# Optimization experiments

Hardware: AMD Instinct MI355X
Metric: run time of the kernel (lower is better)

The kernel has to match this reference:

```python
import jax, jax.numpy as jnp
import numpy as np

B, L, D, H, F, NL, K, G = 2, 2048, 768, 12, 3072, 12, 128, 16
HD = D // H
SCALE = HD ** -0.5


def setup_inputs() -> dict:
    key = jax.random.key(0)
    ks = jax.random.split(key, 8)
    n = lambda k, s, std=0.02: jax.random.normal(k, s, dtype=jnp.float32) * std
    return {
        "x": jax.random.normal(ks[0], (B, L, D), dtype=jnp.float32),
        "pos_conv_w": n(ks[1], (D, D // G, K)),
        "pos_conv_b": jnp.zeros((D,), jnp.float32),
        "ln0_g": jnp.ones((D,), jnp.float32), "ln0_b": jnp.zeros((D,), jnp.float32),
        "Wq": n(ks[2], (NL, D, D)), "bq": jnp.zeros((NL, D), jnp.float32),
        "Wk": n(ks[3], (NL, D, D)), "bk": jnp.zeros((NL, D), jnp.float32),
        "Wv": n(ks[4], (NL, D, D)), "bv": jnp.zeros((NL, D), jnp.float32),
        "Wo": n(ks[5], (NL, D, D)), "bo": jnp.zeros((NL, D), jnp.float32),
        "ln1_g": jnp.ones((NL, D), jnp.float32), "ln1_b": jnp.zeros((NL, D), jnp.float32),
        "W1": n(ks[6], (NL, D, F)), "b1": jnp.zeros((NL, F), jnp.float32),
        "W2": n(ks[7], (NL, F, D)), "b2": jnp.zeros((NL, D), jnp.float32),
        "ln2_g": jnp.ones((NL, D), jnp.float32), "ln2_b": jnp.zeros((NL, D), jnp.float32),
    }


def _ln(x, g, b, eps=1e-5):
    m = jnp.mean(x, axis=-1, keepdims=True)
    v = jnp.mean(jnp.square(x - m), axis=-1, keepdims=True)
    return (x - m) * jax.lax.rsqrt(v + eps) * g + b


def reference(x, pos_conv_w, pos_conv_b, ln0_g, ln0_b, Wq, bq, Wk, bk, Wv, bv, Wo, bo,
              ln1_g, ln1_b, W1, b1, W2, b2, ln2_g, ln2_b):
    b_, l_, d_ = x.shape
    # positional grouped conv embedding (kernel even -> drop last frame), GELU, residual add
    pos = jax.lax.conv_general_dilated(x.transpose(0, 2, 1), pos_conv_w, (1,), [(K // 2, K // 2)],
                                       feature_group_count=G)  # (B, D, L+1)
    pos = pos[:, :, :l_] + pos_conv_b[None, :, None]
    h = x + jax.nn.gelu(pos, approximate=False).transpose(0, 2, 1)
    # post-norm encoder (layer_norm_first=False): LN applied before the layer stack
    h = _ln(h, ln0_g, ln0_b)

    def layer(h, p):
        wq, bq_, wk, bk_, wv, bv_, wo, bo_, g1, be1, w1, bf1, w2, bf2, g2, be2 = p
        r = h
        q = (h @ wq + bq_).reshape(b_, l_, H, HD)
        k = (h @ wk + bk_).reshape(b_, l_, H, HD)
        v = (h @ wv + bv_).reshape(b_, l_, H, HD)
        w = jax.nn.softmax(SCALE * jnp.einsum('blhd,bmhd->bhlm', q, k), axis=-1)
        o = jnp.einsum('bhlm,bmhd->blhd', w, v).reshape(b_, l_, d_)
        h = r + (o @ wo + bo_)
        h = _ln(h, g1, be1)
        ff = jax.nn.gelu(h @ w1 + bf1, approximate=False) @ w2 + bf2
        h = _ln(h + ff, g2, be2)
        return h, None

    h, _ = jax.lax.scan(layer, h, (Wq, bq, Wk, bk, Wv, bv, Wo, bo,
                                   ln1_g, ln1_b, W1, b1, W2, b2, ln2_g, ln2_b))
    return h
```

## Files before the change

### kernel.cpp

```cpp
#include <hip/hip_runtime.h>
#include <hip/hip_bf16.h>
#include <stdint.h>

#define B_ 2
#define L_ 2048
#define D_ 768
#define H_ 12
#define F_ 3072
#define NL_ 12
#define K_ 128
#define G_ 16
#define HD_ 64
#define CPG_ 48
#define M_TOK (B_*L_)
#define SCALE_ 0.125f

typedef __hip_bfloat16 bf16;
typedef __bf16 bf16x8 __attribute__((ext_vector_type(8)));
typedef float f32x4 __attribute__((ext_vector_type(4)));

__device__ __forceinline__ void gload16(const void* g, void* l) {
  __builtin_amdgcn_global_load_lds((const __attribute__((address_space(1))) void*)g,
                                   (__attribute__((address_space(3))) void*)l, 16, 0, 0);
}

__global__ __launch_bounds__(256) void convw_kernel(const float* __restrict__ w,
                                                    bf16* __restrict__ wT2) {
  int idx = blockIdx.x * 256 + threadIdx.x;
  int ci = idx & 63;
  int row = idx >> 6;
  int d = row % 48;
  int t2 = row / 48;
  int kk = t2 & 127;
  int g = t2 >> 7;
  float v = (ci < 48) ? w[(((size_t)(g * 48 + d) * 48) + ci) * 128 + kk] : 0.f;
  wT2[idx] = __float2bfloat16(v);
}

__global__ __launch_bounds__(256) void conv_mfma(const float* __restrict__ x,
                                                 const bf16* __restrict__ wT2,
                                                 const float* __restrict__ bias,
                                                 float* __restrict__ out) {
  int flat = blockIdx.x;
  int wgid = (flat & 7) * 64 + (flat >> 3);
  const int g = wgid >> 5;
  int rem = wgid & 31;
  const int l0 = (rem & 15) * 128;
  const int b = rem >> 4;

  const int tid = threadIdx.x, w = tid >> 6, lane = tid & 63;
  const int c15 = lane & 15, g4 = lane >> 4;
  __shared__ __align__(16) bf16 win[256 * 64];
  __shared__ __align__(16) bf16 Wl[2 * 48 * 64];

  {
    int lg = l0 - 64 + tid;
    char* dst = (char*)win + tid * 128;
    int swr = (tid & 7) << 4;
    uint4 z4 = {0u, 0u, 0u, 0u};
    if ((unsigned)lg < 2048u) {
      const float* srow = x + ((size_t)(b * 2048 + lg) * 768 + g * 48);
#pragma unroll
      for (int c = 0; c < 6; ++c) {
        float4 v0 = *(const float4*)(srow + c * 8);
        float4 v1 = *(const float4*)(srow + c * 8 + 4);
        union { bf16 h[8]; uint4 u; } uu;
        uu.h[0] = __float2bfloat16(v0.x); uu.h[1] = __float2bfloat16(v0.y);
        uu.h[2] = __float2bfloat16(v0.z); uu.h[3] = __float2bfloat16(v0.w);
        uu.h[4] = __float2bfloat16(v1.x); uu.h[5] = __float2bfloat16(v1.y);
        uu.h[6] = __float2bfloat16(v1.z); uu.h[7] = __float2bfloat16(v1.w);
        *(uint4*)(dst + ((c * 16) ^ swr)) = uu.u;
      }
    } else {
#pragma unroll
      for (int c = 0; c < 6; ++c) *(uint4*)(dst + ((c * 16) ^ swr)) = z4;
    }
    *(uint4*)(dst + (96 ^ swr)) = z4;
    *(uint4*)(dst + (112 ^ swr)) = z4;
  }
  __syncthreads();

  f32x4 acc[2][3];
  const f32x4 vzero = {0.f, 0.f, 0.f, 0.f};
#pragma unroll
  for (int i = 0; i < 2; ++i)
#pragma unroll
    for (int j = 0; j < 3; ++j) acc[i][j] = vzero;

  const char* wbase = (const char*)wT2 + (size_t)g * 128 * 48 * 128;

  for (int kp = 0; kp < 64; ++kp) {
#pragma unroll
    for (int i = 0; i < 3; ++i) {
      int coff = w * 3072 + i * 1024;
      int c = coff + (lane << 4);
      int row96 = c >> 7;
      int s = row96 / 48;
      int d = row96 - s * 48;
      int cb2 = c & 127;
      gload16(wbase + ((size_t)((2 * kp + s) * 48 + d)) * 128 + (cb2 ^ ((d & 7) << 4)),
              (char*)Wl + coff);
    }
    __syncthreads();
#pragma unroll
    for (int s = 0; s < 2; ++s) {
      int kk = 2 * kp + s;
#pragma unroll
      for (int cb = 0; cb < 2; ++cb) {
        int a0r = w * 16 + c15 + kk;
        int a1r = 64 + a0r;
        bf16x8 a0 = *(const bf16x8*)((const char*)win + a0r * 128 + ((cb * 64 + g4 * 16) ^ ((a0r & 7) << 4)));
        bf16x8 a1 = *(const bf16x8*)((const char*)win + a1r * 128 + ((cb * 64 + g4 * 16) ^ ((a1r & 7) << 4)));
#pragma unroll
        for (int ct = 0; ct < 3; ++ct) {
          int d = ct * 16 + c15;
          bf16x8 bfrag = *(const bf16x8*)((const char*)Wl + s * 6144 + d * 128 +
                                          ((cb * 64 + g4 * 16) ^ ((d & 7) << 4)));
          acc[0][ct] = __builtin_amdgcn_mfma_f32_16x16x32_bf16(a0, bfrag, acc[0][ct], 0, 0, 0);
          acc[1][ct] = __builtin_amdgcn_mfma_f32_16x16x32_bf16(a1, bfrag, acc[1][ct], 0, 0, 0);
        }
      }
    }
    __syncthreads();
  }

#pragma unroll
  for (int ls = 0; ls < 2; ++ls)
#pragma unroll
    for (int ct = 0; ct < 3; ++ct) {
      int dg = g * 48 + ct * 16 + c15;
      float bv = bias[dg];
#pragma unroll
      for (int r = 0; r < 4; ++r) {
        int l = l0 + ls * 64 + w * 16 + g4 * 4 + r;
        size_t idx = (size_t)(b * 2048 + l) * 768 + dg;
        float vv = acc[ls][ct][r] + bv;
        vv = 0.5f * vv * (1.0f + erff(vv * 0.70710678f));
        out[idx] = x[idx] + vv;
      }
    }
}

__global__ __launch_bounds__(256) void ln_kernel(const float* __restrict__ a,
                                                 const float* __restrict__ r,
                                                 const float* __restrict__ g,
                                                 const float* __restrict__ be,
                                                 float* __restrict__ out,
                                                 bf16* __restrict__ outb) {
  int w = threadIdx.x >> 6, lane = threadIdx.x & 63;
  size_t row = (size_t)blockIdx.x * 4 + w;
  const float* ar = a + row * 768;
  const float* rr = r ? r + row * 768 : nullptr;
  float4 v[3];
  float s = 0.f;
#pragma unroll
  for (int i = 0; i < 3; ++i) {
    int c = lane * 4 + i * 256;
    float4 vv = *(const float4*)(ar + c);
    if (rr) {
      float4 rv = *(const float4*)(rr + c);
      vv.x += rv.x; vv.y += rv.y; vv.z += rv.z; vv.w += rv.w;
    }
    v[i] = vv;
    s += vv.x + vv.y + vv.z + vv.w;
  }
#pragma unroll
  for (int st = 1; st < 64; st <<= 1) s += __shfl_xor(s, st);
  float mean = s * (1.0f / 768.0f);
  float s2 = 0.f;
#pragma unroll
  for (int i = 0; i < 3; ++i) {
    float dx = v[i].x - mean, dy = v[i].y - mean, dz = v[i].z - mean, dw = v[i].w - mean;
    s2 += dx * dx + dy * dy + dz * dz + dw * dw;
  }
#pragma unroll
  for (int st = 1; st < 64; st <<= 1) s2 += __shfl_xor(s2, st);
  float rstd = rsqrtf(s2 * (1.0f / 768.0f) + 1e-5f);
#pragma unroll
  for (int i = 0; i < 3; ++i) {
    int c = lane * 4 + i * 256;
    float4 gv = *(const float4*)(g + c);
    float4 bv = *(const float4*)(be + c);
    float4 ov;
    ov.x = (v[i].x - mean) * rstd * gv.x + bv.x;
    ov.y = (v[i].y - mean) * rstd * gv.y + bv.y;
    ov.z = (v[i].z - mean) * rstd * gv.z + bv.z;
    ov.w = (v[i].w - mean) * rstd * gv.w + bv.w;
    *(float4*)(out + row * 768 + c) = ov;
    if (outb) {
      union { bf16 h[4]; uint2 u; } pk;
      pk.h[0] = __float2bfloat16(ov.x); pk.h[1] = __float2bfloat16(ov.y);
      pk.h[2] = __float2bfloat16(ov.z); pk.h[3] = __float2bfloat16(ov.w);
      *(uint2*)(outb + row * 768 + c) = pk.u;
    }
  }
}

__global__ __launch_bounds__(256) void prep_weights(const float* __restrict__ wq,
                                                    const float* __restrict__ wk,
                                                    const float* __restrict__ wv,
                                                    const float* __restrict__ wo,
                                                    const float* __restrict__ w1,
                                                    const float* __restrict__ w2,
                                                    const float* __restrict__ bq_,
                                                    const float* __restrict__ bk_,
                                                    const float* __restrict__ bv_,
                                                    bf16* __restrict__ wqkvb,
                                                    bf16* __restrict__ wob,
                                                    bf16* __restrict__ w1b,
                                                    bf16* __restrict__ w2b,
                                                    float* __restrict__ bqkv) {
  __shared__ float t[32][33];
  int tid = threadIdx.x;
  int tx = tid & 31, ty = tid >> 5;
  int blk = blockIdx.x;
  if (blk >= 6912) {
    int i = (blk - 6912) * 256 + tid;
    if (i < 2304) bqkv[i] = (i < 768) ? bq_[i] : (i < 1536) ? bk_[i - 768] : bv_[i - 1536];
    return;
  }
  if (blk < 1728) {
    int n0 = (blk % 72) * 32, k0 = (blk / 72) * 32;
    const float* src = (n0 < 768) ? wq : (n0 < 1536) ? wk : wv;
    int nn = (n0 >= 1536) ? (n0 - 1536) : (n0 >= 768 ? n0 - 768 : n0);
#pragma unroll
    for (int i = 0; i < 32; i += 8) t[ty + i][tx] = src[(size_t)(k0 + ty + i) * 768 + nn + tx];
    __syncthreads();
#pragma unroll
    for (int i = 0; i < 32; i += 8)
      wqkvb[(size_t)(n0 + ty + i) * 768 + k0 + tx] = __float2bfloat16(t[tx][ty + i]);
    return;
  }
  blk -= 1728;
  if (blk < 576) {
    int c0 = (blk % 24) * 32, r0 = (blk / 24) * 32;
#pragma unroll
    for (int i = 0; i < 32; i += 8) t[ty + i][tx] = wo[(size_t)(r0 + ty + i) * 768 + c0 + tx];
    __syncthreads();
#pragma unroll
    for (int i = 0; i < 32; i += 8)
      wob[(size_t)(c0 + ty + i) * 768 + r0 + tx] = __float2bfloat16(t[tx][ty + i]);
    return;
  }
  blk -= 576;
  if (blk < 2304) {
    int c0 = (blk % 96) * 32, r0 = (blk / 96) * 32;
#pragma unroll
    for (int i = 0; i < 32; i += 8) t[ty + i][tx] = w1[(size_t)(r0 + ty + i) * 3072 + c0 + tx];
    __syncthreads();
#pragma unroll
    for (int i = 0; i < 32; i += 8)
      w1b[(size_t)(c0 + ty + i) * 768 + r0 + tx] = __float2bfloat16(t[tx][ty + i]);
    return;
  }
  blk -= 2304;
  {
    int c0 = (blk % 24) * 32, r0 = (blk / 24) * 32;
#pragma unroll
    for (int i = 0; i < 32; i += 8) t[ty + i][tx] = w2[(size_t)(r0 + ty + i) * 768 + c0 + tx];
    __syncthreads();
#pragma unroll
    for (int i = 0; i < 32; i += 8)
      w2b[(size_t)(c0 + ty + i) * 3072 + r0 + tx] = __float2bfloat16(t[tx][ty + i]);
  }
}

template <int BM, int BN, int GELU, int BF16OUT, int VOUT = 0>
__global__ __launch_bounds__(256) void gemm_bf16(const bf16* __restrict__ A,
                                                 const bf16* __restrict__ BT,
                                                 const float* __restrict__ bias,
                                                 void* __restrict__ Cout,
                                                 int N, int Kd,
                                                 bf16* __restrict__ vTout = nullptr) {
  constexpr int WM = BM / 2, MF = WM / 16;
  constexpr int WN = BN / 2, FN = WN / 16;
  __shared__ bf16 As[BM * 64];
  __shared__ bf16 Bs[BN * 64];
  const int tid = threadIdx.x, w = tid >> 6, lane = tid & 63;
  int gx = gridDim.x;
  int flat = blockIdx.x + gx * blockIdx.y;
  int cpx = (gx * gridDim.y) >> 3;
  int sw = (flat & 7) * cpx + (flat >> 3);
  const int bn = sw % gx, bm = sw / gx;
  const int wr = w >> 1, wc = w & 1;
  const int c15 = lane & 15, g4 = lane >> 4;
  const int lrow8 = lane >> 3;
  const int cb = (lane & 7) * 16;

  f32x4 acc[MF][FN];
  const f32x4 vzero = {0.f, 0.f, 0.f, 0.f};
#pragma unroll
  for (int i = 0; i < MF; ++i)
#pragma unroll
    for (int j = 0; j < FN; ++j) acc[i][j] = vzero;

  const char* Ab = (const char*)A;
  const char* Bb = (const char*)BT;

  for (int k0 = 0; k0 < Kd; k0 += 64) {
#pragma unroll
    for (int i = 0; i < BM / 32; ++i) {
      int t = w + 4 * i;
      int row = t * 8 + lrow8;
      gload16(Ab + ((size_t)(bm * BM + row) * Kd + k0) * 2 + (cb ^ ((row & 7) << 4)),
              (char*)As + t * 1024);
    }
#pragma unroll
    for (int i = 0; i < BN / 32; ++i) {
      int t = w + 4 * i;
      int row = t * 8 + lrow8;
      gload16(Bb + ((size_t)(bn * BN + row) * Kd + k0) * 2 + (cb ^ ((row & 7) << 4)),
              (char*)Bs + t * 1024);
    }
    __syncthreads();
    bf16x8 af[MF][2], bfr[FN][2];
#pragma unroll
    for (int kf = 0; kf < 2; ++kf) {
      int kbyte = kf * 64 + g4 * 16;
#pragma unroll
      for (int mf = 0; mf < MF; ++mf) {
        int row = wr * WM + mf * 16 + c15;
        af[mf][kf] = *(const bf16x8*)((const char*)As + row * 128 + (kbyte ^ ((row & 7) << 4)));
      }
#pragma unroll
      for (int fn = 0; fn < FN; ++fn) {
        int row = wc * WN + fn * 16 + c15;
        bfr[fn][kf] = *(const bf16x8*)((const char*)Bs + row * 128 + (kbyte ^ ((row & 7) << 4)));
      }
    }
    __builtin_amdgcn_s_setprio(1);
#pragma unroll
    for (int mf = 0; mf < MF; ++mf)
#pragma unroll
      for (int fn = 0; fn < FN; ++fn) {
        acc[mf][fn] = __builtin_amdgcn_mfma_f32_16x16x32_bf16(af[mf][0], bfr[fn][0], acc[mf][fn], 0, 0, 0);
        acc[mf][fn] = __builtin_amdgcn_mfma_f32_16x16x32_bf16(af[mf][1], bfr[fn][1], acc[mf][fn], 0, 0, 0);
      }
    __builtin_amdgcn_s_setprio(0);
    __syncthreads();
  }
#pragma unroll
  for (int fn = 0; fn < FN; ++fn) {
    int col = bn * BN + wc * WN + fn * 16 + c15;
    float bv = bias[col];
#pragma unroll
    for (int mf = 0; mf < MF; ++mf) {
#pragma unroll
      for (int r = 0; r < 4; ++r) {
        int row = bm * BM + wr * WM + mf * 16 + g4 * 4 + r;
        float vv = acc[mf][fn][r] + bv;
        if (GELU) vv = 0.5f * vv * (1.0f + erff(vv * 0.70710678f));
        if (BF16OUT) {
          if (VOUT && col >= 1536) {
            int hd2 = col - 1536, hh = hd2 >> 6, dd = hd2 & 63;
            int bb = row >> 11, ll = row & 2047;
            vTout[((size_t)((bb * 12 + hh) * 64 + dd) << 11) + ll] = __float2bfloat16(vv);
          } else {
            ((bf16*)Cout)[(size_t)row * N + col] = __float2bfloat16(vv);
          }
        } else {
          ((float*)Cout)[(size_t)row * N + col] = vv;
        }
      }
    }
  }
}

__global__ __launch_bounds__(256) void attn_mfma(const bf16* __restrict__ qkv,
                                                 const bf16* __restrict__ vT,
                                                 bf16* __restrict__ ob) {
  int bid = blockIdx.x + 32 * (blockIdx.y + 12 * blockIdx.z);
  int wgid = (bid & 7) * 96 + (bid >> 3);
  const int q0 = (wgid & 31) * 64;
  int bh = wgid >> 5;
  const int h = bh % 12, b = bh / 12;

  const int tid = threadIdx.x, w = tid >> 6, lane = tid & 63;
  const int c15 = lane & 15, g4 = lane >> 4;
  const int lrow8 = lane >> 3;
  const int cb = (lane & 7) * 16;
  __shared__ bf16 Kl[2][4096];
  __shared__ bf16 Vl[2][4096];
  __shared__ bf16 Pl[4096];

  const f32x4 vzero = {0.f, 0.f, 0.f, 0.f};
  const char* qp = (const char*)qkv + (((size_t)(b * 2048 + q0 + w * 16 + c15)) * 2304 + h * 64) * 2;
  bf16x8 qa0 = *(const bf16x8*)(qp + g4 * 16);
  bf16x8 qa1 = *(const bf16x8*)(qp + 64 + g4 * 16);

  bf16x8 b_one;
#pragma unroll
  for (int i = 0; i < 8; ++i) b_one[i] = (__bf16)1.0f;

  f32x4 o[4], o5;
#pragma unroll
  for (int i = 0; i < 4; ++i) o[i] = vzero;
  o5 = vzero;
  float m = -1e30f;
  const float SC2 = 0.18033688f;
  const float THR = 11.54f;

  const char* kgb = (const char*)qkv + (((size_t)(b * 2048)) * 2304 + 768 + h * 64) * 2;
  const char* vgb = (const char*)vT + ((size_t)((b * 12 + h) * 64) * 2048) * 2;
  char* Plw = (char*)Pl + w * 2048;

#define STAGE(kt, bufi)                                                                     \
  {                                                                                         \
    char* Kd = (char*)Kl[bufi];                                                             \
    char* Vd = (char*)Vl[bufi];                                                             \
    _Pragma("unroll")                                                                       \
    for (int i = 0; i < 2; ++i) {                                                           \
      int t = w + 4 * i;                                                                    \
      int rr = t * 8 + lrow8;                                                               \
      gload16(kgb + (size_t)((kt) * 64 + rr) * 4608 + (cb ^ ((rr & 7) << 4)), Kd + t * 1024);\
      gload16(vgb + (size_t)rr * 4096 + (size_t)(kt) * 128 + (cb ^ ((rr & 7) << 4)), Vd + t * 1024);\
    }                                                                                       \
  }

  STAGE(0, 0);
  __syncthreads();

  for (int kt = 0; kt < 32; ++kt) {
    int cur = kt & 1;
    if (kt + 1 < 32) STAGE(kt + 1, cur ^ 1);

    const char* Kc = (const char*)Kl[cur];
    const char* Vc = (const char*)Vl[cur];

    f32x4 sc[4];
    __builtin_amdgcn_s_setprio(1);
#pragma unroll
    for (int fn = 0; fn < 4; ++fn) {
      int key = fn * 16 + c15;
      const char* kr = Kc + key * 128;
      int sw = (key & 7) << 4;
      bf16x8 kb0 = *(const bf16x8*)(kr + ((g4 * 16) ^ sw));
      bf16x8 kb1 = *(const bf16x8*)(kr + ((64 + g4 * 16) ^ sw));
      f32x4 s = __builtin_amdgcn_mfma_f32_16x16x32_bf16(kb0, qa0, vzero, 0, 0, 0);
      s = __builtin_amdgcn_mfma_f32_16x16x32_bf16(kb1, qa1, s, 0, 0, 0);
      sc[fn] = s;
    }
    __builtin_amdgcn_s_setprio(0);

    float pm = fmaxf(
        fmaxf(fmaxf(fmaxf(sc[0][0], sc[0][1]), fmaxf(sc[0][2], sc[0][3])),
              fmaxf(fmaxf(sc[1][0], sc[1][1]), fmaxf(sc[1][2], sc[1][3]))),
        fmaxf(fmaxf(fmaxf(sc[2][0], sc[2][1]), fmaxf(sc[2][2], sc[2][3])),
              fmaxf(fmaxf(sc[3][0], sc[3][1]), fmaxf(sc[3][2], sc[3][3]))));
    int ok = (pm * SC2 <= m + THR) ? 1 : 0;

    if (!__all(ok)) {
      float tm = pm;
      tm = fmaxf(tm, __shfl_xor(tm, 16));
      tm = fmaxf(tm, __shfl_xor(tm, 32));
      float mn = fmaxf(m, tm * SC2);
      float alpha = exp2f(m - mn);
      m = mn;
#pragma unroll
      for (int r = 0; r < 4; ++r) {
        float ar = __shfl(alpha, g4 * 4 + r);
        o[0][r] *= ar; o[1][r] *= ar; o[2][r] *= ar; o[3][r] *= ar;
        o5[r] *= ar;
      }
    }

    {
      char* prow = Plw + c15 * 128;
      int swp = (c15 & 7) << 4;
#pragma unroll
      for (int fn = 0; fn < 4; ++fn) {
        union { bf16 hh[4]; uint2 u; } pk;
#pragma unroll
        for (int r = 0; r < 4; ++r)
          pk.hh[r] = __float2bfloat16(exp2f(fmaf(sc[fn][r], SC2, -m)));
        *(uint2*)(prow + ((fn * 32 + g4 * 8) ^ swp)) = pk.u;
      }
    }

    {
      const char* pr = Plw + c15 * 128;
      int sw = (c15 & 7) << 4;
      bf16x8 pa0 = *(const bf16x8*)(pr + ((g4 * 16) ^ sw));
      bf16x8 pa1 = *(const bf16x8*)(pr + ((64 + g4 * 16) ^ sw));
      __builtin_amdgcn_s_setprio(1);
#pragma unroll
      for (int fh = 0; fh < 4; ++fh) {
        int hd = fh * 16 + c15;
        const char* vr = Vc + hd * 128;
        int swv = (hd & 7) << 4;
        bf16x8 vb0 = *(const bf16x8*)(vr + ((g4 * 16) ^ swv));
        bf16x8 vb1 = *(const bf16x8*)(vr + ((64 + g4 * 16) ^ swv));
        o[fh] = __builtin_amdgcn_mfma_f32_16x16x32_bf16(pa0, vb0, o[fh], 0, 0, 0);
        o[fh] = __builtin_amdgcn_mfma_f32_16x16x32_bf16(pa1, vb1, o[fh], 0, 0, 0);
      }
      o5 = __builtin_amdgcn_mfma_f32_16x16x32_bf16(pa0, b_one, o5, 0, 0, 0);
      o5 = __builtin_amdgcn_mfma_f32_16x16x32_bf16(pa1, b_one, o5, 0, 0, 0);
      __builtin_amdgcn_s_setprio(0);
    }
    __syncthreads();
  }
#undef STAGE

#pragma unroll
  for (int r = 0; r < 4; ++r) {
    float inv = 1.0f / o5[r];
    size_t row = (size_t)(b * 2048 + q0 + w * 16 + g4 * 4 + r);
#pragma unroll
    for (int fh = 0; fh < 4; ++fh)
      ob[row * 768 + h * 64 + fh * 16 + c15] = __float2bfloat16(o[fh][r] * inv);
  }
}

extern "C" void kernel_launch(void* const* d_in, const int* in_sizes, int n_in,
                              void* d_out, int out_size, void* d_ws, size_t ws_size,
                              hipStream_t stream) {
  const float* x      = (const float*)d_in[0];
  const float* pcw    = (const float*)d_in[1];
  const float* pcb    = (const float*)d_in[2];
  const float* ln0_g  = (const float*)d_in[3];
  const float* ln0_b  = (const float*)d_in[4];
  const float* Wq     = (const float*)d_in[5];
  const float* bq     = (const float*)d_in[6];
  const float* Wk     = (const float*)d_in[7];
  const float* bk     = (const float*)d_in[8];
  const float* Wv     = (const float*)d_in[9];
  const float* bv     = (const float*)d_in[10];
  const float* Wo     = (const float*)d_in[11];
  const float* bo     = (const float*)d_in[12];
  const float* ln1_g  = (const float*)d_in[13];
  const float* ln1_b  = (const float*)d_in[14];
  const float* W1     = (const float*)d_in[15];
  const float* b1     = (const float*)d_in[16];
  const float* W2     = (const float*)d_in[17];
  const float* b2     = (const float*)d_in[18];
  const float* ln2_g  = (const float*)d_in[19];
  const float* ln2_b  = (const float*)d_in[20];

  const size_t MDB = (size_t)M_TOK * D_ * 4;
  char* W = (char*)d_ws;
  float* h    = (float*)W;
  float* tmp  = (float*)(W + MDB);
  char*  big  = W + 2 * MDB;
  bf16*  qkv  = (bf16*)big;
  bf16*  ff   = (bf16*)big;
  bf16*  wT2  = (bf16*)big;
  char* p = W + 2 * MDB + 25165824;
  bf16* h_bf  = (bf16*)p; p += (size_t)M_TOK * D_ * 2;
  bf16* obuf  = (bf16*)p; p += (size_t)M_TOK * D_ * 2;
  bf16* vT    = (bf16*)p; p += (size_t)M_TOK * D_ * 2;
  bf16* wqkvb = (bf16*)p; p += (size_t)2304 * 768 * 2;
  bf16* wob   = (bf16*)p; p += (size_t)768 * 768 * 2;
  bf16* w1b   = (bf16*)p; p += (size_t)3072 * 768 * 2;
  bf16* w2b   = (bf16*)p; p += (size_t)768 * 3072 * 2;
  float* bqkv = (float*)p;

  convw_kernel<<<24576, 256, 0, stream>>>(pcw, wT2);
  conv_mfma<<<512, 256, 0, stream>>>(x, wT2, pcb, tmp);
  ln_kernel<<<M_TOK / 4, 256, 0, stream>>>(tmp, nullptr, ln0_g, ln0_b, h, h_bf);

  for (int l = 0; l < NL_; ++l) {
    const float* wq = Wq + (size_t)l * D_ * D_;
    const float* wk = Wk + (size_t)l * D_ * D_;
    const float* wv = Wv + (size_t)l * D_ * D_;
    const float* wo = Wo + (size_t)l * D_ * D_;
    const float* w1 = W1 + (size_t)l * D_ * F_;
    const float* w2 = W2 + (size_t)l * F_ * D_;

    prep_weights<<<6921, 256, 0, stream>>>(wq, wk, wv, wo, w1, w2,
                                           bq + (size_t)l * D_, bk + (size_t)l * D_, bv + (size_t)l * D_,
                                           wqkvb, wob, w1b, w2b, bqkv);

    gemm_bf16<128, 128, 0, 1, 1><<<dim3(18, 32), 256, 0, stream>>>(h_bf, wqkvb, bqkv, qkv, 2304, 768, vT);
    attn_mfma<<<dim3(32, 12, 2), 256, 0, stream>>>(qkv, vT, obuf);
    gemm_bf16<64, 64, 0, 0><<<dim3(12, 64), 256, 0, stream>>>(obuf, wob, bo + (size_t)l * D_, tmp, 768, 768);
    ln_kernel<<<M_TOK / 4, 256, 0, stream>>>(tmp, h, ln1_g + (size_t)l * D_, ln1_b + (size_t)l * D_, h, h_bf);
    gemm_bf16<128, 128, 1, 1><<<dim3(24, 32), 256, 0, stream>>>(h_bf, w1b, b1 + (size_t)l * F_, ff, 3072, 768);
    gemm_bf16<64, 64, 0, 0><<<dim3(12, 64), 256, 0, stream>>>(ff, w2b, b2 + (size_t)l * D_, tmp, 768, 3072);
    float* out_ln2 = (l == NL_ - 1) ? (float*)d_out : h;
    ln_kernel<<<M_TOK / 4, 256, 0, stream>>>(tmp, h, ln2_g + (size_t)l * D_, ln2_b + (size_t)l * D_, out_ln2, h_bf);
  }
}
```

Before: 2.403 ms.

## Split attention keys across wave pairs and batch weight prep for all layers

The attention kernel now has each wave handle 32 query rows over half of the key tiles (even or odd). It uses a 4-deep K/V shared-memory ring and merges the two partial softmax states through shared memory at the end. This gives more MFMA work per K/V fragment load and more independent work per wave, at the cost of more registers and a final cross-wave reduction. Separately, the per-layer weight conversion and transposition is hoisted into a single 12-layer launch when the workspace is large enough, which removes eleven launches and lets the conversion run as one larger grid.

Result: slower. 2.684 ms (+11.7%).

```diff
diff --git a/kernel.cpp b/kernel.cpp
--- a/kernel.cpp
+++ b/kernel.cpp
@@ -196,27 +196,45 @@
   }
 }
 
-__global__ __launch_bounds__(256) void prep_weights(const float* __restrict__ wq,
-                                                    const float* __restrict__ wk,
-                                                    const float* __restrict__ wv,
-                                                    const float* __restrict__ wo,
-                                                    const float* __restrict__ w1,
-                                                    const float* __restrict__ w2,
-                                                    const float* __restrict__ bq_,
-                                                    const float* __restrict__ bk_,
-                                                    const float* __restrict__ bv_,
-                                                    bf16* __restrict__ wqkvb,
-                                                    bf16* __restrict__ wob,
-                                                    bf16* __restrict__ w1b,
-                                                    bf16* __restrict__ w2b,
-                                                    float* __restrict__ bqkv) {
+__global__ __launch_bounds__(256) void prep_weights(const float* __restrict__ WqB,
+                                                    const float* __restrict__ WkB,
+                                                    const float* __restrict__ WvB,
+                                                    const float* __restrict__ WoB,
+                                                    const float* __restrict__ W1B,
+                                                    const float* __restrict__ W2B,
+                                                    const float* __restrict__ bqB,
+                                                    const float* __restrict__ bkB,
+                                                    const float* __restrict__ bvB,
+                                                    bf16* __restrict__ wqkvbA,
+                                                    bf16* __restrict__ wobA,
+                                                    bf16* __restrict__ w1bA,
+                                                    bf16* __restrict__ w2bA,
+                                                    float* __restrict__ bqkvA,
+                                                    int lstart) {
   __shared__ float t[32][33];
   int tid = threadIdx.x;
   int tx = tid & 31, ty = tid >> 5;
+  int ly = blockIdx.y;
+  int l = lstart + ly;
+  const float* wq = WqB + (size_t)l * 768 * 768;
+  const float* wk = WkB + (size_t)l * 768 * 768;
+  const float* wv = WvB + (size_t)l * 768 * 768;
+  const float* wo = WoB + (size_t)l * 768 * 768;
+  const float* w1 = W1B + (size_t)l * 768 * 3072;
+  const float* w2 = W2B + (size_t)l * 3072 * 768;
+  bf16* wqkvb = wqkvbA + (size_t)ly * 2304 * 768;
+  bf16* wob   = wobA + (size_t)ly * 768 * 768;
+  bf16* w1b   = w1bA + (size_t)ly * 3072 * 768;
+  bf16* w2b   = w2bA + (size_t)ly * 768 * 3072;
+  float* bqkv = bqkvA + (size_t)ly * 2304;
+
   int blk = blockIdx.x;
   if (blk >= 6912) {
     int i = (blk - 6912) * 256 + tid;
-    if (i < 2304) bqkv[i] = (i < 768) ? bq_[i] : (i < 1536) ? bk_[i - 768] : bv_[i - 1536];
+    if (i < 2304)
+      bqkv[i] = (i < 768) ? bqB[(size_t)l * 768 + i]
+              : (i < 1536) ? bkB[(size_t)l * 768 + i - 768]
+                           : bvB[(size_t)l * 768 + i - 1536];
     return;
   }
   if (blk < 1728) {
@@ -376,38 +394,43 @@
   const int h = bh % 12, b = bh / 12;
 
   const int tid = threadIdx.x, w = tid >> 6, lane = tid & 63;
+  const int p = w >> 1, qh = w & 1;
   const int c15 = lane & 15, g4 = lane >> 4;
   const int lrow8 = lane >> 3;
   const int cb = (lane & 7) * 16;
-  __shared__ bf16 Kl[2][4096];
-  __shared__ bf16 Vl[2][4096];
-  __shared__ bf16 Pl[4096];
+  __shared__ bf16 Kl[4][4096];
+  __shared__ bf16 Vl[4][4096];
+  __shared__ bf16 Pl[4][2048];
 
   const f32x4 vzero = {0.f, 0.f, 0.f, 0.f};
-  const char* qp = (const char*)qkv + (((size_t)(b * 2048 + q0 + w * 16 + c15)) * 2304 + h * 64) * 2;
-  bf16x8 qa0 = *(const bf16x8*)(qp + g4 * 16);
-  bf16x8 qa1 = *(const bf16x8*)(qp + 64 + g4 * 16);
-
+  bf16x8 qa[2][2];
+#pragma unroll
+  for (int qt = 0; qt < 2; ++qt) {
+    const char* qp = (const char*)qkv +
+        (((size_t)(b * 2048 + q0 + qh * 32 + qt * 16 + c15)) * 2304 + h * 64) * 2;
+    qa[qt][0] = *(const bf16x8*)(qp + g4 * 16);
+    qa[qt][1] = *(const bf16x8*)(qp + 64 + g4 * 16);
+  }
   bf16x8 b_one;
 #pragma unroll
   for (int i = 0; i < 8; ++i) b_one[i] = (__bf16)1.0f;
 
-  f32x4 o[4], o5;
-#pragma unroll
-  for (int i = 0; i < 4; ++i) o[i] = vzero;
-  o5 = vzero;
-  float m = -1e30f;
+  f32x4 o[4][2], o5[2];
+#pragma unroll
+  for (int i = 0; i < 4; ++i) { o[i][0] = vzero; o[i][1] = vzero; }
+  o5[0] = vzero; o5[1] = vzero;
+  float m[2] = {-1e30f, -1e30f};
   const float SC2 = 0.18033688f;
   const float THR = 11.54f;
 
   const char* kgb = (const char*)qkv + (((size_t)(b * 2048)) * 2304 + 768 + h * 64) * 2;
   const char* vgb = (const char*)vT + ((size_t)((b * 12 + h) * 64) * 2048) * 2;
-  char* Plw = (char*)Pl + w * 2048;
-
-#define STAGE(kt, bufi)                                                                     \
+  char* Plw = (char*)Pl + w * 4096;
+
+#define STAGET(kt)                                                                          \
   {                                                                                         \
-    char* Kd = (char*)Kl[bufi];                                                             \
-    char* Vd = (char*)Vl[bufi];                                                             \
+    char* Kd = (char*)Kl[(kt) & 3];                                                         \
+    char* Vd = (char*)Vl[(kt) & 3];                                                         \
     _Pragma("unroll")                                                                       \
     for (int i = 0; i < 2; ++i) {                                                           \
       int t = w + 4 * i;                                                                    \
@@ -417,71 +440,88 @@
     }                                                                                       \
   }
 
-  STAGE(0, 0);
+  STAGET(0); STAGET(1);
   __syncthreads();
 
-  for (int kt = 0; kt < 32; ++kt) {
-    int cur = kt & 1;
-    if (kt + 1 < 32) STAGE(kt + 1, cur ^ 1);
-
-    const char* Kc = (const char*)Kl[cur];
-    const char* Vc = (const char*)Vl[cur];
-
-    f32x4 sc[4];
+  for (int j = 0; j < 16; ++j) {
+    if (j < 15) { STAGET(2 * j + 2); STAGET(2 * j + 3); }
+    int kt = 2 * j + p;
+    const char* Kc = (const char*)Kl[kt & 3];
+    const char* Vc = (const char*)Vl[kt & 3];
+
+    f32x4 sc[4][2];
     __builtin_amdgcn_s_setprio(1);
 #pragma unroll
     for (int fn = 0; fn < 4; ++fn) {
       int key = fn * 16 + c15;
       const char* kr = Kc + key * 128;
-      int sw = (key & 7) << 4;
-      bf16x8 kb0 = *(const bf16x8*)(kr + ((g4 * 16) ^ sw));
-      bf16x8 kb1 = *(const bf16x8*)(kr + ((64 + g4 * 16) ^ sw));
-      f32x4 s = __builtin_amdgcn_mfma_f32_16x16x32_bf16(kb0, qa0, vzero, 0, 0, 0);
-      s = __builtin_amdgcn_mfma_f32_16x16x32_bf16(kb1, qa1, s, 0, 0, 0);
-      sc[fn] = s;
+      int swk = (key & 7) << 4;
+      bf16x8 kb0 = *(const bf16x8*)(kr + ((g4 * 16) ^ swk));
+      bf16x8 kb1 = *(const bf16x8*)(kr + ((64 + g4 * 16) ^ swk));
+#pragma unroll
+      for (int qt = 0; qt < 2; ++qt) {
+        f32x4 s = __builtin_amdgcn_mfma_f32_16x16x32_bf16(kb0, qa[qt][0], vzero, 0, 0, 0);
+        s = __builtin_amdgcn_mfma_f32_16x16x32_bf16(kb1, qa[qt][1], s, 0, 0, 0);
+        sc[fn][qt] = s;
+      }
     }
     __builtin_amdgcn_s_setprio(0);
 
-    float pm = fmaxf(
-        fmaxf(fmaxf(fmaxf(sc[0][0], sc[0][1]), fmaxf(sc[0][2], sc[0][3])),
-              fmaxf(fmaxf(sc[1][0], sc[1][1]), fmaxf(sc[1][2], sc[1][3]))),
-        fmaxf(fmaxf(fmaxf(sc[2][0], sc[2][1]), fmaxf(sc[2][2], sc[2][3])),
-              fmaxf(fmaxf(sc[3][0], sc[3][1]), fmaxf(sc[3][2], sc[3][3]))));
-    int ok = (pm * SC2 <= m + THR) ? 1 : 0;
+    float pm[2];
+    int ok = 1;
+#pragma unroll
+    for (int qt = 0; qt < 2; ++qt) {
+      pm[qt] = fmaxf(
+          fmaxf(fmaxf(fmaxf(sc[0][qt][0], sc[0][qt][1]), fmaxf(sc[0][qt][2], sc[0][qt][3])),
+                fmaxf(fmaxf(sc[1][qt][0], sc[1][qt][1]), fmaxf(sc[1][qt][2], sc[1][qt][3]))),
+          fmaxf(fmaxf(fmaxf(sc[2][qt][0], sc[2][qt][1]), fmaxf(sc[2][qt][2], sc[2][qt][3])),
+                fmaxf(fmaxf(sc[3][qt][0], sc[3][qt][1]), fmaxf(sc[3][qt][2], sc[3][qt][3]))));
+      ok &= (pm[qt] * SC2 <= m[qt] + THR) ? 1 : 0;
+    }
 
     if (!__all(ok)) {
-      float tm = pm;
-      tm = fmaxf(tm, __shfl_xor(tm, 16));
-      tm = fmaxf(tm, __shfl_xor(tm, 32));
-      float mn = fmaxf(m, tm * SC2);
-      float alpha = exp2f(m - mn);
-      m = mn;
-#pragma unroll
-      for (int r = 0; r < 4; ++r) {
-        float ar = __shfl(alpha, g4 * 4 + r);
-        o[0][r] *= ar; o[1][r] *= ar; o[2][r] *= ar; o[3][r] *= ar;
-        o5[r] *= ar;
-      }
-    }
-
-    {
-      char* prow = Plw + c15 * 128;
+#pragma unroll
+      for (int qt = 0; qt < 2; ++qt) {
+        float tm = pm[qt];
+        tm = fmaxf(tm, __shfl_xor(tm, 16));
+        tm = fmaxf(tm, __shfl_xor(tm, 32));
+        float mn = fmaxf(m[qt], tm * SC2);
+        float alpha = exp2f(m[qt] - mn);
+        m[qt] = mn;
+#pragma unroll
+        for (int r = 0; r < 4; ++r) {
+          float ar = __shfl(alpha, g4 * 4 + r);
+          o[0][qt][r] *= ar; o[1][qt][r] *= ar; o[2][qt][r] *= ar; o[3][qt][r] *= ar;
+          o5[qt][r] *= ar;
+        }
+      }
+    }
+
+#pragma unroll
+    for (int qt = 0; qt < 2; ++qt) {
+      int ro = qt * 16 + c15;
+      char* prow = Plw + ro * 128;
       int swp = (c15 & 7) << 4;
 #pragma unroll
       for (int fn = 0; fn < 4; ++fn) {
         union { bf16 hh[4]; uint2 u; } pk;
 #pragma unroll
         for (int r = 0; r < 4; ++r)
-          pk.hh[r] = __float2bfloat16(exp2f(fmaf(sc[fn][r], SC2, -m)));
+          pk.hh[r] = __float2bfloat16(exp2f(fmaf(sc[fn][qt][r], SC2, -m[qt])));
         *(uint2*)(prow + ((fn * 32 + g4 * 8) ^ swp)) = pk.u;
       }
     }
 
     {
-      const char* pr = Plw + c15 * 128;
-      int sw = (c15 & 7) << 4;
-      bf16x8 pa0 = *(const bf16x8*)(pr + ((g4 * 16) ^ sw));
-      bf16x8 pa1 = *(const bf16x8*)(pr + ((64 + g4 * 16) ^ sw));
+      bf16x8 pa[2][2];
+#pragma unroll
+      for (int qt = 0; qt < 2; ++qt) {
+        int ro = qt * 16 + c15;
+        const char* pr = Plw + ro * 128;
+        int swp = (c15 & 7) << 4;
+        pa[qt][0] = *(const bf16x8*)(pr + ((g4 * 16) ^ swp));
+        pa[qt][1] = *(const bf16x8*)(pr + ((64 + g4 * 16) ^ swp));
+      }
       __builtin_amdgcn_s_setprio(1);
 #pragma unroll
       for (int fh = 0; fh < 4; ++fh) {
@@ -490,24 +530,61 @@
         int swv = (hd & 7) << 4;
         bf16x8 vb0 = *(const bf16x8*)(vr + ((g4 * 16) ^ swv));
         bf16x8 vb1 = *(const bf16x8*)(vr + ((64 + g4 * 16) ^ swv));
-        o[fh] = __builtin_amdgcn_mfma_f32_16x16x32_bf16(pa0, vb0, o[fh], 0, 0, 0);
-        o[fh] = __builtin_amdgcn_mfma_f32_16x16x32_bf16(pa1, vb1, o[fh], 0, 0, 0);
-      }
-      o5 = __builtin_amdgcn_mfma_f32_16x16x32_bf16(pa0, b_one, o5, 0, 0, 0);
-      o5 = __builtin_amdgcn_mfma_f32_16x16x32_bf16(pa1, b_one, o5, 0, 0, 0);
+#pragma unroll
+        for (int qt = 0; qt < 2; ++qt) {
+          o[fh][qt] = __builtin_amdgcn_mfma_f32_16x16x32_bf16(pa[qt][0], vb0, o[fh][qt], 0, 0, 0);
+          o[fh][qt] = __builtin_amdgcn_mfma_f32_16x16x32_bf16(pa[qt][1], vb1, o[fh][qt], 0, 0, 0);
+        }
+      }
+#pragma unroll
+      for (int qt = 0; qt < 2; ++qt) {
+        o5[qt] = __builtin_amdgcn_mfma_f32_16x16x32_bf16(pa[qt][0], b_one, o5[qt], 0, 0, 0);
+        o5[qt] = __builtin_amdgcn_mfma_f32_16x16x32_bf16(pa[qt][1], b_one, o5[qt], 0, 0, 0);
+      }
       __builtin_amdgcn_s_setprio(0);
     }
     __syncthreads();
   }
-#undef STAGE
-
-#pragma unroll
-  for (int r = 0; r < 4; ++r) {
-    float inv = 1.0f / o5[r];
-    size_t row = (size_t)(b * 2048 + q0 + w * 16 + g4 * 4 + r);
-#pragma unroll
-    for (int fh = 0; fh < 4; ++fh)
-      ob[row * 768 + h * 64 + fh * 16 + c15] = __float2bfloat16(o[fh][r] * inv);
+#undef STAGET
+
+  float* Obuf  = (float*)Kl;
+  float* o5buf = (float*)Vl;
+  float* mbuf  = (float*)Vl + 64;
+  if (p == 1) {
+#pragma unroll
+    for (int qt = 0; qt < 2; ++qt) {
+      if (g4 == 0) mbuf[qh * 32 + qt * 16 + c15] = m[qt];
+#pragma unroll
+      for (int r = 0; r < 4; ++r) {
+        int ql = qt * 16 + g4 * 4 + r;
+        if (c15 == 0) o5buf[qh * 32 + ql] = o5[qt][r];
+#pragma unroll
+        for (int fh = 0; fh < 4; ++fh)
+          Obuf[(size_t)(qh * 32 + ql) * 64 + fh * 16 + c15] = o[fh][qt][r];
+      }
+    }
+  }
+  __syncthreads();
+  if (p == 0) {
+#pragma unroll
+    for (int qt = 0; qt < 2; ++qt) {
+#pragma unroll
+      for (int r = 0; r < 4; ++r) {
+        int ql = qt * 16 + g4 * 4 + r;
+        float m1 = mbuf[qh * 32 + ql];
+        float m0r = __shfl(m[qt], g4 * 4 + r);
+        float mf = fmaxf(m0r, m1);
+        float a0 = exp2f(m0r - mf), a1 = exp2f(m1 - mf);
+        float lsum = o5[qt][r] * a0 + o5buf[qh * 32 + ql] * a1;
+        float inv = 1.0f / lsum;
+        size_t row = (size_t)(b * 2048 + q0 + qh * 32 + ql);
+#pragma unroll
+        for (int fh = 0; fh < 4; ++fh) {
+          float val = o[fh][qt][r] * a0 + Obuf[(size_t)(qh * 32 + ql) * 64 + fh * 16 + c15] * a1;
+          ob[row * 768 + h * 64 + fh * 16 + c15] = __float2bfloat16(val * inv);
+        }
+      }
+    }
   }
 }
 
@@ -548,27 +625,40 @@
   bf16* h_bf  = (bf16*)p; p += (size_t)M_TOK * D_ * 2;
   bf16* obuf  = (bf16*)p; p += (size_t)M_TOK * D_ * 2;
   bf16* vT    = (bf16*)p; p += (size_t)M_TOK * D_ * 2;
-  bf16* wqkvb = (bf16*)p; p += (size_t)2304 * 768 * 2;
-  bf16* wob   = (bf16*)p; p += (size_t)768 * 768 * 2;
-  bf16* w1b   = (bf16*)p; p += (size_t)3072 * 768 * 2;
-  bf16* w2b   = (bf16*)p; p += (size_t)768 * 3072 * 2;
-  float* bqkv = (float*)p;
+
+  const size_t S_QKV = (size_t)2304 * 768;
+  const size_t S_WO  = (size_t)768 * 768;
+  const size_t S_W1  = (size_t)3072 * 768;
+  const size_t S_W2  = (size_t)768 * 3072;
+  size_t base_off = (size_t)(p - W);
+  size_t need = base_off + 12 * (S_QKV + S_WO + S_W1 + S_W2) * 2 + 12 * 2304 * 4;
+  int hoist = (ws_size >= need) ? 1 : 0;
+  int NL_prep = hoist ? 12 : 1;
+
+  bf16* wqkvbA = (bf16*)p; p += S_QKV * 2 * NL_prep;
+  bf16* wobA   = (bf16*)p; p += S_WO * 2 * NL_prep;
+  bf16* w1bA   = (bf16*)p; p += S_W1 * 2 * NL_prep;
+  bf16* w2bA   = (bf16*)p; p += S_W2 * 2 * NL_prep;
+  float* bqkvA = (float*)p;
 
   convw_kernel<<<24576, 256, 0, stream>>>(pcw, wT2);
   conv_mfma<<<512, 256, 0, stream>>>(x, wT2, pcb, tmp);
   ln_kernel<<<M_TOK / 4, 256, 0, stream>>>(tmp, nullptr, ln0_g, ln0_b, h, h_bf);
 
+  if (hoist)
+    prep_weights<<<dim3(6921, 12), 256, 0, stream>>>(Wq, Wk, Wv, Wo, W1, W2, bq, bk, bv,
+                                                     wqkvbA, wobA, w1bA, w2bA, bqkvA, 0);
+
   for (int l = 0; l < NL_; ++l) {
-    const float* wq = Wq + (size_t)l * D_ * D_;
-    const float* wk = Wk + (size_t)l * D_ * D_;
-    const float* wv = Wv + (size_t)l * D_ * D_;
-    const float* wo = Wo + (size_t)l * D_ * D_;
-    const float* w1 = W1 + (size_t)l * D_ * F_;
-    const float* w2 = W2 + (size_t)l * F_ * D_;
-
-    prep_weights<<<6921, 256, 0, stream>>>(wq, wk, wv, wo, w1, w2,
-                                           bq + (size_t)l * D_, bk + (size_t)l * D_, bv + (size_t)l * D_,
-                                           wqkvb, wob, w1b, w2b, bqkv);
+    if (!hoist)
+      prep_weights<<<dim3(6921, 1), 256, 0, stream>>>(Wq, Wk, Wv, Wo, W1, W2, bq, bk, bv,
+                                                      wqkvbA, wobA, w1bA, w2bA, bqkvA, l);
+    int li = hoist ? l : 0;
+    bf16* wqkvb = wqkvbA + (size_t)li * S_QKV;
+    bf16* wob   = wobA + (size_t)li * S_WO;
+    bf16* w1b   = w1bA + (size_t)li * S_W1;
+    bf16* w2b   = w2bA + (size_t)li * S_W2;
+    float* bqkv = bqkvA + (size_t)li * 2304;
 
     gemm_bf16<128, 128, 0, 1, 1><<<dim3(18, 32), 256, 0, stream>>>(h_bf, wqkvb, bqkv, qkv, 2304, 768, vT);
     attn_mfma<<<dim3(32, 12, 2), 256, 0, stream>>>(qkv, vT, obuf);
```
